# Kernel optimization log

Hardware: AMD Instinct MI355X
Metric: run time of the kernel (lower is better)

## Reference

```python
import jax, jax.numpy as jnp
import numpy as np

B, S, E, H = 32, 512, 512, 8
D = E // H  # head dim = 64
EPS = 1e-5


def setup_inputs() -> dict:
    key = jax.random.key(0)
    ks = jax.random.split(key, 6)
    x = jax.random.normal(ks[0], (B, S, E), dtype=jnp.float32)
    # nn.MultiheadAttention packed in-projection: [3E, E] weight, [3E] bias
    w_in = jax.random.normal(ks[1], (3 * E, E), dtype=jnp.float32) * 0.02
    b_in = jnp.zeros((3 * E,), dtype=jnp.float32)
    # out_proj: Linear(E, E)
    w_out = jax.random.normal(ks[2], (E, E), dtype=jnp.float32) * 0.02
    b_out = jnp.zeros((E,), dtype=jnp.float32)
    # LayerNorm(E) affine params
    gamma = jnp.ones((E,), dtype=jnp.float32)
    beta = jnp.zeros((E,), dtype=jnp.float32)
    return {"x": x, "w_in": w_in, "b_in": b_in, "w_out": w_out,
            "b_out": b_out, "gamma": gamma, "beta": beta}


def reference(x, w_in, b_in, w_out, b_out, gamma, beta):
    b, s, e = x.shape
    # packed QKV projection (torch: x @ W^T + b)
    qkv = x @ w_in.T + b_in                      # [B, S, 3E]
    q, k, v = jnp.split(qkv, 3, axis=-1)         # each [B, S, E]
    def to_heads(t):
        return t.reshape(b, s, H, D).transpose(0, 2, 1, 3)  # [B, H, S, D]
    q, k, v = to_heads(q), to_heads(k), to_heads(v)
    scores = jnp.einsum("bhqd,bhkd->bhqk", q, k) / jnp.sqrt(jnp.float32(D))
    att_w = jax.nn.softmax(scores, axis=-1)      # [B, H, S, S] per-head weights
    z = jnp.einsum("bhqk,bhkd->bhqd", att_w, v)  # [B, H, S, D]
    z = z.transpose(0, 2, 1, 3).reshape(b, s, e) # merge heads
    z = z @ w_out.T + b_out                      # out projection
    z = z + x                                    # residual connection
    # LayerNorm over last dim
    mu = jnp.mean(z, axis=-1, keepdims=True)
    var = jnp.var(z, axis=-1, keepdims=True)
    y = (z - mu) * jax.lax.rsqrt(var + EPS) * gamma + beta
    return (y, att_w)
```

## Files before the change

kernel.cpp:

```cpp
#include <hip/hip_runtime.h>
#include <hip/hip_bf16.h>
#include <stdint.h>

#define Bb 32
#define Ss 512
#define Ee 512
#define Hh 8
#define Dd 64
#define EPSf 1e-5f

typedef __attribute__((ext_vector_type(8))) unsigned short ushort8_t;
typedef __attribute__((ext_vector_type(4))) unsigned short ushort4_t;
typedef __attribute__((ext_vector_type(4))) float f32x4;
typedef __attribute__((ext_vector_type(4))) unsigned int uint4_t;
typedef __attribute__((ext_vector_type(8))) __bf16 bf16x8;

union U8cast { ushort8_t u; bf16x8 b; uint4_t w; };
__device__ __forceinline__ bf16x8 as_bf16x8(ushort8_t u) { U8cast c; c.u = u; return c.b; }
__device__ __forceinline__ bf16x8 words_bf16x8(unsigned int w0, unsigned int w1,
                                               unsigned int w2, unsigned int w3) {
  U8cast c; c.w = (uint4_t){w0, w1, w2, w3}; return c.b;
}

__device__ __forceinline__ unsigned short f2bf(float f) {
  __bf16 b = (__bf16)f;
  return __builtin_bit_cast(unsigned short, b);
}
__device__ __forceinline__ unsigned int pack2bf(float lo, float hi) {
  return ((unsigned int)f2bf(hi) << 16) | f2bf(lo);
}

__device__ __forceinline__ f32x4 mfma16(bf16x8 a, bf16x8 b, f32x4 c) {
  return __builtin_amdgcn_mfma_f32_16x16x32_bf16(a, b, c, 0, 0, 0);
}

__device__ __forceinline__ void async16(const unsigned short* g, unsigned short* l) {
  __builtin_amdgcn_global_load_lds(
      (const __attribute__((address_space(1))) void*)g,
      (__attribute__((address_space(3))) void*)l, 16, 0, 0);
}

__global__ __launch_bounds__(256) void cvt_bf16(const float* __restrict__ src,
                                                unsigned short* __restrict__ dst, int n8) {
  int i = blockIdx.x * 256 + threadIdx.x;
  int stride = gridDim.x * 256;
  for (; i < n8; i += stride) {
    float4 v0 = ((const float4*)src)[2 * i];
    float4 v1 = ((const float4*)src)[2 * i + 1];
    ushort8_t o;
    o[0] = f2bf(v0.x); o[1] = f2bf(v0.y); o[2] = f2bf(v0.z); o[3] = f2bf(v0.w);
    o[4] = f2bf(v1.x); o[5] = f2bf(v1.y); o[6] = f2bf(v1.z); o[7] = f2bf(v1.w);
    ((ushort8_t*)dst)[i] = o;
  }
}

__global__ __launch_bounds__(256) void qkv_mm(
    const unsigned short* __restrict__ Xb, const unsigned short* __restrict__ Wb,
    const float* __restrict__ bin,
    unsigned short* __restrict__ QL, unsigned short* __restrict__ KL,
    unsigned short* __restrict__ VL) {
  __shared__ unsigned short SH[128 * 128];
  unsigned short* As = SH;
  unsigned short* Bs = SH + 128 * 64;
  const int tid = threadIdx.x;
  const int w = tid >> 6, l = tid & 63;
  const int lr = l & 15, lg = l >> 4;
  const int id = blockIdx.x;
  const int gid = (id & 7) * 192 + (id >> 3);
  const int bx = gid % 12, by = gid / 12;
  const int m0 = by * 128, n0 = bx * 128;
  const int wm = (w >> 1) * 64, wn = (w & 1) * 64;
  f32x4 acc[4][4];
#pragma unroll
  for (int i = 0; i < 4; ++i)
#pragma unroll
    for (int j = 0; j < 4; ++j) acc[i][j] = (f32x4){0.f, 0.f, 0.f, 0.f};

  for (int k0 = 0; k0 < 512; k0 += 64) {
#pragma unroll
    for (int i = 0; i < 4; ++i) {
      int ci = (w * 4 + i) * 64 + l;
      int row = ci >> 3, kc = ci & 7;
      int gkc = kc ^ (row & 7);
      async16(Xb + (size_t)(m0 + row) * 512 + k0 + gkc * 8, &As[(w * 4 + i) * 512]);
      async16(Wb + (size_t)(n0 + row) * 512 + k0 + gkc * 8, &Bs[(w * 4 + i) * 512]);
    }
    __syncthreads();
#pragma unroll
    for (int ks = 0; ks < 2; ++ks) {
      bf16x8 af[4], bfr[4];
#pragma unroll
      for (int mf = 0; mf < 4; ++mf) {
        int row = wm + mf * 16 + lr;
        int gc = ks * 4 + lg;
        af[mf] = as_bf16x8(*(const ushort8_t*)&As[row * 64 + ((gc ^ (row & 7)) * 8)]);
      }
#pragma unroll
      for (int nf = 0; nf < 4; ++nf) {
        int row = wn + nf * 16 + lr;
        int gc = ks * 4 + lg;
        bfr[nf] = as_bf16x8(*(const ushort8_t*)&Bs[row * 64 + ((gc ^ (row & 7)) * 8)]);
      }
#pragma unroll
      for (int mf = 0; mf < 4; ++mf)
#pragma unroll
        for (int nf = 0; nf < 4; ++nf) acc[mf][nf] = mfma16(af[mf], bfr[nf], acc[mf][nf]);
    }
    __syncthreads();
  }

  const int which = n0 >> 9;
  const int bb = m0 >> 9, s0b = m0 & 511;
  const int h0 = (n0 & 511) >> 6;
#pragma unroll
  for (int nf = 0; nf < 4; ++nf) {
    int nl = wn + nf * 16 + lr;
    float bias = bin[n0 + nl];
#pragma unroll
    for (int mf = 0; mf < 4; ++mf) {
#pragma unroll
      for (int r = 0; r < 4; ++r) {
        int ml = wm + mf * 16 + lg * 4 + r;
        int row = (which == 2) ? nl : ml;
        int col = (which == 2) ? ml : nl;
        SH[row * 128 + ((((col >> 3) ^ (row & 7)) << 3) | (col & 7))] =
            f2bf(acc[mf][nf][r] + bias);
      }
    }
  }
  __syncthreads();

  unsigned short* dst = (which == 0) ? QL : (which == 1) ? KL : VL;
  const int frag0 = s0b >> 3;
#pragma unroll
  for (int i = 0; i < 8; ++i) {
    int c = tid + i * 256;
    int h_rel = c >> 10, cc = c & 1023;
    int fr = cc >> 6, ln = cc & 63;
    int row, col;
    if (which == 0) {
      row = (fr >> 1) * 16 + (ln & 15);
      col = h_rel * 64 + (fr & 1) * 32 + (ln >> 4) * 8;
    } else if (which == 1) {
      row = (fr >> 2) * 32 + ((fr >> 1) & 1) * 4 + ((ln & 15) >> 2) * 8 + (ln & 3);
      col = h_rel * 64 + (fr & 1) * 32 + (ln >> 4) * 8;
    } else {
      row = h_rel * 64 + (fr & 3) * 16 + (ln & 15);
      col = (fr >> 2) * 32 + (ln >> 4) * 8;
    }
    ushort8_t v = *(const ushort8_t*)&SH[row * 128 + (((col >> 3) ^ (row & 7)) << 3)];
    size_t base = (size_t)(bb * Hh + h0 + h_rel) * 32768;
    *(ushort8_t*)&dst[base + (size_t)(frag0 + fr) * 512 + ln * 8] = v;
  }
}

__global__ __launch_bounds__(256, 4) void attn_fused(
    const unsigned short* __restrict__ QL, const unsigned short* __restrict__ KL,
    const unsigned short* __restrict__ VL, float* __restrict__ att,
    unsigned short* __restrict__ Zb) {
  __shared__ unsigned short SH[2][8192];
  const int tid = threadIdx.x;
  const int w = tid >> 6, l = tid & 63;
  const int lr = l & 15, lg = l >> 4;
  const int id = blockIdx.x;
  const int bh = (id >> 6) * 8 + (id & 7);
  const int m0 = ((id >> 3) & 7) * 64;
  const int b = bh >> 3, h = bh & 7;
  const unsigned short* Qp = QL + (size_t)bh * 32768;
  const unsigned short* Kp = KL + (size_t)bh * 32768;
  const unsigned short* Vp = VL + (size_t)bh * 32768;

  const int qb = (m0 >> 4) + w;
  bf16x8 bq0 = as_bf16x8(*(const ushort8_t*)(Qp + (size_t)(qb * 2) * 512 + l * 8));
  bf16x8 bq1 = as_bf16x8(*(const ushort8_t*)(Qp + (size_t)(qb * 2 + 1) * 512 + l * 8));

#define STAGE_K(C, buf)                                                        \
  {                                                                            \
    _Pragma("unroll") for (int i = 0; i < 2; ++i)                              \
        async16(Kp + (size_t)(C)*4096 + (w * 2 + i) * 512 + l * 8,             \
                &SH[buf][(w * 2 + i) * 512]);                                  \
  }
#define STAGE_V(C, buf)                                                        \
  {                                                                            \
    _Pragma("unroll") for (int i = 0; i < 2; ++i)                              \
        async16(Vp + (size_t)(C)*4096 + (w * 2 + i) * 512 + l * 8,             \
                &SH[buf][4096 + (w * 2 + i) * 512]);                           \
  }

  float m_run = -1e30f, ssum = 0.f;
  STAGE_K(0, 0);
  __syncthreads();
#pragma unroll
  for (int C = 0; C < 8; ++C) {
    if (C < 7) STAGE_K(C + 1, (C + 1) & 1);
    f32x4 s4[4];
#pragma unroll
    for (int j = 0; j < 4; ++j) {
      bf16x8 ak0 = as_bf16x8(*(const ushort8_t*)&SH[C & 1][(2 * j) * 512 + l * 8]);
      bf16x8 ak1 = as_bf16x8(*(const ushort8_t*)&SH[C & 1][(2 * j + 1) * 512 + l * 8]);
      f32x4 z = (f32x4){0.f, 0.f, 0.f, 0.f};
      z = mfma16(ak0, bq0, z);
      s4[j] = mfma16(ak1, bq1, z);
    }
    float cm = s4[0][0];
#pragma unroll
    for (int j = 0; j < 4; ++j)
#pragma unroll
      for (int r = 0; r < 4; ++r) cm = fmaxf(cm, s4[j][r]);
    cm = fmaxf(cm, __shfl_xor(cm, 16));
    cm = fmaxf(cm, __shfl_xor(cm, 32));
    float nm = fmaxf(m_run, cm);
    ssum *= __expf((m_run - nm) * 0.125f);
    m_run = nm;
#pragma unroll
    for (int j = 0; j < 4; ++j) {
      float p0 = __expf((s4[j][0] - nm) * 0.125f);
      float p1 = __expf((s4[j][1] - nm) * 0.125f);
      float p2 = __expf((s4[j][2] - nm) * 0.125f);
      float p3 = __expf((s4[j][3] - nm) * 0.125f);
      ssum += (p0 + p1) + (p2 + p3);
    }
    __syncthreads();
  }
  ssum += __shfl_xor(ssum, 16);
  ssum += __shfl_xor(ssum, 32);
  const float inv = 1.0f / ssum;
  const float mfin = m_run;

  f32x4 o[4];
#pragma unroll
  for (int df = 0; df < 4; ++df) o[df] = (f32x4){0.f, 0.f, 0.f, 0.f};
  float* attb = att + (size_t)bh * Ss * Ss + (size_t)(m0 + w * 16) * Ss;
  const int dr8 = l >> 3, dc = l & 7;
  const int src0 = ((dc >> 1) << 4) + dr8;
  const int podd = dc & 1;

  STAGE_K(0, 0);
  STAGE_V(0, 0);
  __syncthreads();
#pragma unroll
  for (int C = 0; C < 8; ++C) {
    if (C < 7) {
      STAGE_K(C + 1, (C + 1) & 1);
      STAGE_V(C + 1, (C + 1) & 1);
    }
    f32x4 s4[4];
#pragma unroll
    for (int j = 0; j < 4; ++j) {
      bf16x8 ak0 = as_bf16x8(*(const ushort8_t*)&SH[C & 1][(2 * j) * 512 + l * 8]);
      bf16x8 ak1 = as_bf16x8(*(const ushort8_t*)&SH[C & 1][(2 * j + 1) * 512 + l * 8]);
      f32x4 z = (f32x4){0.f, 0.f, 0.f, 0.f};
      z = mfma16(ak0, bq0, z);
      s4[j] = mfma16(ak1, bq1, z);
    }
#pragma unroll
    for (int j = 0; j < 4; ++j)
#pragma unroll
      for (int r = 0; r < 4; ++r)
        s4[j][r] = __expf((s4[j][r] - mfin) * 0.125f) * inv;

#pragma unroll
    for (int cc = 0; cc < 2; ++cc) {
      int c2 = 2 * C + cc;
#pragma unroll
      for (int hh = 0; hh < 2; ++hh) {
        int srcl = src0 + hh * 8;
        f32x4 g;
        g[0] = __shfl(s4[2 * cc + podd][0], srcl, 64);
        g[1] = __shfl(s4[2 * cc + podd][1], srcl, 64);
        g[2] = __shfl(s4[2 * cc + podd][2], srcl, 64);
        g[3] = __shfl(s4[2 * cc + podd][3], srcl, 64);
        float* p = attb + (size_t)(hh * 8 + dr8) * Ss + c2 * 32 + dc * 4;
        __builtin_nontemporal_store(g, (f32x4*)p);
      }
      bf16x8 bp = words_bf16x8(pack2bf(s4[2 * cc][0], s4[2 * cc][1]),
                               pack2bf(s4[2 * cc][2], s4[2 * cc][3]),
                               pack2bf(s4[2 * cc + 1][0], s4[2 * cc + 1][1]),
                               pack2bf(s4[2 * cc + 1][2], s4[2 * cc + 1][3]));
#pragma unroll
      for (int df = 0; df < 4; ++df) {
        bf16x8 av = as_bf16x8(
            *(const ushort8_t*)&SH[C & 1][4096 + (cc * 4 + df) * 512 + l * 8]);
        o[df] = mfma16(av, bp, o[df]);
      }
    }
    __syncthreads();
  }

  unsigned short* zrow = Zb + ((size_t)(b * Ss) + m0 + w * 16 + lr) * Ee + h * Dd;
#pragma unroll
  for (int df = 0; df < 4; ++df) {
    ushort4_t zz;
    zz[0] = f2bf(o[df][0]); zz[1] = f2bf(o[df][1]);
    zz[2] = f2bf(o[df][2]); zz[3] = f2bf(o[df][3]);
    *(ushort4_t*)(zrow + df * 16 + lg * 4) = zz;
  }
#undef STAGE_K
#undef STAGE_V
}

__global__ __launch_bounds__(256) void out_mm(
    const unsigned short* __restrict__ Zb, const unsigned short* __restrict__ Wb,
    const float* __restrict__ bout, const float* __restrict__ X,
    float* __restrict__ Y) {
  __shared__ unsigned short As[128 * 64];
  __shared__ unsigned short Bs[128 * 64];
  const int tid = threadIdx.x;
  const int w = tid >> 6, l = tid & 63;
  const int lr = l & 15, lg = l >> 4;
  const int id = blockIdx.x;
  const int gid = (id & 7) * 64 + (id >> 3);
  const int m0 = (gid >> 2) * 128, n0 = (gid & 3) * 128;
  const int wm = (w >> 1) * 64, wn = (w & 1) * 64;
  f32x4 acc[4][4];
#pragma unroll
  for (int i = 0; i < 4; ++i)
#pragma unroll
    for (int j = 0; j < 4; ++j) acc[i][j] = (f32x4){0.f, 0.f, 0.f, 0.f};

  for (int k0 = 0; k0 < 512; k0 += 64) {
#pragma unroll
    for (int i = 0; i < 4; ++i) {
      int ci = (w * 4 + i) * 64 + l;
      int row = ci >> 3, kc = ci & 7;
      int gkc = kc ^ (row & 7);
      async16(Zb + (size_t)(m0 + row) * 512 + k0 + gkc * 8, &As[(w * 4 + i) * 512]);
      async16(Wb + (size_t)(n0 + row) * 512 + k0 + gkc * 8, &Bs[(w * 4 + i) * 512]);
    }
    __syncthreads();
#pragma unroll
    for (int ks = 0; ks < 2; ++ks) {
      bf16x8 af[4], bfr[4];
#pragma unroll
      for (int mf = 0; mf < 4; ++mf) {
        int row = wm + mf * 16 + lr;
        int gc = ks * 4 + lg;
        af[mf] = as_bf16x8(*(const ushort8_t*)&As[row * 64 + ((gc ^ (row & 7)) * 8)]);
      }
#pragma unroll
      for (int nf = 0; nf < 4; ++nf) {
        int row = wn + nf * 16 + lr;
        int gc = ks * 4 + lg;
        bfr[nf] = as_bf16x8(*(const ushort8_t*)&Bs[row * 64 + ((gc ^ (row & 7)) * 8)]);
      }
#pragma unroll
      for (int mf = 0; mf < 4; ++mf)
#pragma unroll
        for (int nf = 0; nf < 4; ++nf) acc[mf][nf] = mfma16(af[mf], bfr[nf], acc[mf][nf]);
    }
    __syncthreads();
  }

#pragma unroll
  for (int nf = 0; nf < 4; ++nf) {
    int n = n0 + wn + nf * 16 + lr;
    float bias = bout[n];
#pragma unroll
    for (int mf = 0; mf < 4; ++mf) {
#pragma unroll
      for (int r = 0; r < 4; ++r) {
        int m = m0 + wm + mf * 16 + lg * 4 + r;
        Y[(size_t)m * 512 + n] = acc[mf][nf][r] + bias + X[(size_t)m * 512 + n];
      }
    }
  }
}

__global__ __launch_bounds__(128) void ln_kernel(
    const float* __restrict__ Z2, const float* __restrict__ gamma,
    const float* __restrict__ beta, float* __restrict__ Y) {
  const int row = blockIdx.x;
  const int t = threadIdx.x;
  float4 v = *(const float4*)(Z2 + (size_t)row * 512 + t * 4);
  float sum = v.x + v.y + v.z + v.w;
  float sq = v.x * v.x + v.y * v.y + v.z * v.z + v.w * v.w;
#pragma unroll
  for (int off = 32; off; off >>= 1) {
    sum += __shfl_xor(sum, off);
    sq += __shfl_xor(sq, off);
  }
  __shared__ float s0[2], s1[2];
  int wv = t >> 6;
  if ((t & 63) == 0) { s0[wv] = sum; s1[wv] = sq; }
  __syncthreads();
  sum = s0[0] + s0[1];
  sq = s1[0] + s1[1];
  float mu = sum * (1.0f / 512.0f);
  float var = sq * (1.0f / 512.0f) - mu * mu;
  float rs = rsqrtf(var + EPSf);
  float4 g = *(const float4*)(gamma + t * 4);
  float4 be = *(const float4*)(beta + t * 4);
  float4 o;
  o.x = (v.x - mu) * rs * g.x + be.x;
  o.y = (v.y - mu) * rs * g.y + be.y;
  o.z = (v.z - mu) * rs * g.z + be.z;
  o.w = (v.w - mu) * rs * g.w + be.w;
  *(float4*)(Y + (size_t)row * 512 + t * 4) = o;
}

extern "C" void kernel_launch(void* const* d_in, const int* in_sizes, int n_in,
                              void* d_out, int out_size, void* d_ws, size_t ws_size,
                              hipStream_t stream) {
  const float* x = (const float*)d_in[0];
  const float* w_in = (const float*)d_in[1];
  const float* b_in = (const float*)d_in[2];
  const float* w_out = (const float*)d_in[3];
  const float* b_out = (const float*)d_in[4];
  const float* gamma = (const float*)d_in[5];
  const float* beta = (const float*)d_in[6];

  float* y = (float*)d_out;
  float* att = (float*)d_out + (size_t)Bb * Ss * Ee;

  char* ws = (char*)d_ws;
  const size_t NBH = (size_t)Bb * Hh * Ss * Dd;
  unsigned short* QLb   = (unsigned short*)ws;
  unsigned short* KLb   = QLb + NBH;
  unsigned short* VLb   = KLb + NBH;
  unsigned short* xb    = VLb + NBH;
  unsigned short* Zb    = xb;
  unsigned short* winb  = xb + NBH;
  unsigned short* woutb = winb + (size_t)3 * Ee * Ee;

  cvt_bf16<<<dim3(1024), 256, 0, stream>>>(x, xb, (int)(NBH / 8));
  cvt_bf16<<<dim3(384), 256, 0, stream>>>(w_in, winb, (int)(3 * Ee * Ee / 8));
  cvt_bf16<<<dim3(128), 256, 0, stream>>>(w_out, woutb, (int)(Ee * Ee / 8));
  qkv_mm<<<dim3(1536), 256, 0, stream>>>(xb, winb, b_in, QLb, KLb, VLb);
  attn_fused<<<dim3(2048), 256, 0, stream>>>(QLb, KLb, VLb, att, Zb);
  out_mm<<<dim3(512), 256, 0, stream>>>(Zb, woutb, b_out, x, y);
  ln_kernel<<<dim3(16384), 128, 0, stream>>>(y, gamma, beta, y);
}
```

Measured before the change: 169.2 us.

## Fuse LayerNorm into out-projection GEMM and merge conversion kernels

```diff
diff --git a/kernel.cpp b/kernel.cpp
--- a/kernel.cpp
+++ b/kernel.cpp
@@ -40,13 +40,22 @@
       (__attribute__((address_space(3))) void*)l, 16, 0, 0);
 }
 
-__global__ __launch_bounds__(256) void cvt_bf16(const float* __restrict__ src,
-                                                unsigned short* __restrict__ dst, int n8) {
+__global__ __launch_bounds__(256) void cvt_all(
+    const float* __restrict__ x, const float* __restrict__ win,
+    const float* __restrict__ wout, unsigned short* __restrict__ dst) {
+  const int NX = 1048576;
+  const int NW = 98304;
+  const int NT = NX + NW + 32768;
   int i = blockIdx.x * 256 + threadIdx.x;
   int stride = gridDim.x * 256;
-  for (; i < n8; i += stride) {
-    float4 v0 = ((const float4*)src)[2 * i];
-    float4 v1 = ((const float4*)src)[2 * i + 1];
+  for (; i < NT; i += stride) {
+    const float* s;
+    int off;
+    if (i < NX) { s = x; off = i; }
+    else if (i < NX + NW) { s = win; off = i - NX; }
+    else { s = wout; off = i - NX - NW; }
+    float4 v0 = ((const float4*)s)[2 * off];
+    float4 v1 = ((const float4*)s)[2 * off + 1];
     ushort8_t o;
     o[0] = f2bf(v0.x); o[1] = f2bf(v0.y); o[2] = f2bf(v0.z); o[3] = f2bf(v0.w);
     o[4] = f2bf(v1.x); o[5] = f2bf(v1.y); o[6] = f2bf(v1.z); o[7] = f2bf(v1.w);
@@ -299,103 +308,128 @@
 #undef STAGE_V
 }
 
-__global__ __launch_bounds__(256) void out_mm(
+__global__ __launch_bounds__(256) void out_ln(
     const unsigned short* __restrict__ Zb, const unsigned short* __restrict__ Wb,
     const float* __restrict__ bout, const float* __restrict__ X,
+    const float* __restrict__ gamma, const float* __restrict__ beta,
     float* __restrict__ Y) {
-  __shared__ unsigned short As[128 * 64];
-  __shared__ unsigned short Bs[128 * 64];
+  __shared__ unsigned short As[32 * 32];
+  __shared__ unsigned short Bs[512 * 32];
   const int tid = threadIdx.x;
   const int w = tid >> 6, l = tid & 63;
   const int lr = l & 15, lg = l >> 4;
   const int id = blockIdx.x;
   const int gid = (id & 7) * 64 + (id >> 3);
-  const int m0 = (gid >> 2) * 128, n0 = (gid & 3) * 128;
-  const int wm = (w >> 1) * 64, wn = (w & 1) * 64;
-  f32x4 acc[4][4];
-#pragma unroll
-  for (int i = 0; i < 4; ++i)
-#pragma unroll
-    for (int j = 0; j < 4; ++j) acc[i][j] = (f32x4){0.f, 0.f, 0.f, 0.f};
-
-  for (int k0 = 0; k0 < 512; k0 += 64) {
-#pragma unroll
-    for (int i = 0; i < 4; ++i) {
-      int ci = (w * 4 + i) * 64 + l;
-      int row = ci >> 3, kc = ci & 7;
-      int gkc = kc ^ (row & 7);
-      async16(Zb + (size_t)(m0 + row) * 512 + k0 + gkc * 8, &As[(w * 4 + i) * 512]);
-      async16(Wb + (size_t)(n0 + row) * 512 + k0 + gkc * 8, &Bs[(w * 4 + i) * 512]);
-    }
-    __syncthreads();
-#pragma unroll
-    for (int ks = 0; ks < 2; ++ks) {
-      bf16x8 af[4], bfr[4];
-#pragma unroll
-      for (int mf = 0; mf < 4; ++mf) {
-        int row = wm + mf * 16 + lr;
-        int gc = ks * 4 + lg;
-        af[mf] = as_bf16x8(*(const ushort8_t*)&As[row * 64 + ((gc ^ (row & 7)) * 8)]);
-      }
-#pragma unroll
-      for (int nf = 0; nf < 4; ++nf) {
-        int row = wn + nf * 16 + lr;
-        int gc = ks * 4 + lg;
-        bfr[nf] = as_bf16x8(*(const ushort8_t*)&Bs[row * 64 + ((gc ^ (row & 7)) * 8)]);
-      }
-#pragma unroll
-      for (int mf = 0; mf < 4; ++mf)
-#pragma unroll
-        for (int nf = 0; nf < 4; ++nf) acc[mf][nf] = mfma16(af[mf], bfr[nf], acc[mf][nf]);
-    }
-    __syncthreads();
-  }
-
-#pragma unroll
-  for (int nf = 0; nf < 4; ++nf) {
-    int n = n0 + wn + nf * 16 + lr;
+  const int m0 = gid * 32;
+  const int wn = w * 128;
+  f32x4 acc[2][8];
+#pragma unroll
+  for (int i = 0; i < 2; ++i)
+#pragma unroll
+    for (int j = 0; j < 8; ++j) acc[i][j] = (f32x4){0.f, 0.f, 0.f, 0.f};
+
+  for (int k0 = 0; k0 < 512; k0 += 32) {
+#pragma unroll
+    for (int i = 0; i < 8; ++i) {
+      int ci = tid + i * 256;
+      int row = ci >> 2, kc = ci & 3, gkc = kc ^ (row & 3);
+      async16(Wb + (size_t)row * 512 + k0 + gkc * 8, &Bs[ci * 8]);
+    }
+    if (tid < 128) {
+      int row = tid >> 2, kc = tid & 3, gkc = kc ^ (row & 3);
+      async16(Zb + (size_t)(m0 + row) * 512 + k0 + gkc * 8, &As[tid * 8]);
+    }
+    __syncthreads();
+    bf16x8 af[2], bfr[8];
+#pragma unroll
+    for (int mf = 0; mf < 2; ++mf) {
+      int row = mf * 16 + lr;
+      af[mf] = as_bf16x8(*(const ushort8_t*)&As[row * 32 + ((lg ^ (row & 3)) * 8)]);
+    }
+#pragma unroll
+    for (int nf = 0; nf < 8; ++nf) {
+      int row = wn + nf * 16 + lr;
+      bfr[nf] = as_bf16x8(*(const ushort8_t*)&Bs[row * 32 + ((lg ^ (row & 3)) * 8)]);
+    }
+#pragma unroll
+    for (int mf = 0; mf < 2; ++mf)
+#pragma unroll
+      for (int nf = 0; nf < 8; ++nf) acc[mf][nf] = mfma16(af[mf], bfr[nf], acc[mf][nf]);
+    __syncthreads();
+  }
+
+  float sum[2][4], sq[2][4];
+#pragma unroll
+  for (int mf = 0; mf < 2; ++mf)
+#pragma unroll
+    for (int r = 0; r < 4; ++r) { sum[mf][r] = 0.f; sq[mf][r] = 0.f; }
+#pragma unroll
+  for (int nf = 0; nf < 8; ++nf) {
+    int n = wn + nf * 16 + lr;
     float bias = bout[n];
 #pragma unroll
-    for (int mf = 0; mf < 4; ++mf) {
+    for (int mf = 0; mf < 2; ++mf)
 #pragma unroll
       for (int r = 0; r < 4; ++r) {
-        int m = m0 + wm + mf * 16 + lg * 4 + r;
-        Y[(size_t)m * 512 + n] = acc[mf][nf][r] + bias + X[(size_t)m * 512 + n];
-      }
-    }
-  }
-}
-
-__global__ __launch_bounds__(128) void ln_kernel(
-    const float* __restrict__ Z2, const float* __restrict__ gamma,
-    const float* __restrict__ beta, float* __restrict__ Y) {
-  const int row = blockIdx.x;
-  const int t = threadIdx.x;
-  float4 v = *(const float4*)(Z2 + (size_t)row * 512 + t * 4);
-  float sum = v.x + v.y + v.z + v.w;
-  float sq = v.x * v.x + v.y * v.y + v.z * v.z + v.w * v.w;
-#pragma unroll
-  for (int off = 32; off; off >>= 1) {
-    sum += __shfl_xor(sum, off);
-    sq += __shfl_xor(sq, off);
-  }
-  __shared__ float s0[2], s1[2];
-  int wv = t >> 6;
-  if ((t & 63) == 0) { s0[wv] = sum; s1[wv] = sq; }
+        int m = m0 + mf * 16 + lg * 4 + r;
+        float v = acc[mf][nf][r] + bias + X[(size_t)m * 512 + n];
+        acc[mf][nf][r] = v;
+        sum[mf][r] += v;
+        sq[mf][r] += v * v;
+      }
+  }
+#pragma unroll
+  for (int mask = 1; mask < 16; mask <<= 1) {
+#pragma unroll
+    for (int mf = 0; mf < 2; ++mf)
+#pragma unroll
+      for (int r = 0; r < 4; ++r) {
+        sum[mf][r] += __shfl_xor(sum[mf][r], mask);
+        sq[mf][r] += __shfl_xor(sq[mf][r], mask);
+      }
+  }
+  float* S = (float*)As;
+  if (lr == 0) {
+#pragma unroll
+    for (int mf = 0; mf < 2; ++mf)
+#pragma unroll
+      for (int r = 0; r < 4; ++r) {
+        int row = mf * 16 + lg * 4 + r;
+        S[(w * 32 + row) * 2] = sum[mf][r];
+        S[(w * 32 + row) * 2 + 1] = sq[mf][r];
+      }
+  }
   __syncthreads();
-  sum = s0[0] + s0[1];
-  sq = s1[0] + s1[1];
-  float mu = sum * (1.0f / 512.0f);
-  float var = sq * (1.0f / 512.0f) - mu * mu;
-  float rs = rsqrtf(var + EPSf);
-  float4 g = *(const float4*)(gamma + t * 4);
-  float4 be = *(const float4*)(beta + t * 4);
-  float4 o;
-  o.x = (v.x - mu) * rs * g.x + be.x;
-  o.y = (v.y - mu) * rs * g.y + be.y;
-  o.z = (v.z - mu) * rs * g.z + be.z;
-  o.w = (v.w - mu) * rs * g.w + be.w;
-  *(float4*)(Y + (size_t)row * 512 + t * 4) = o;
+  float musv[2][4], rssv[2][4];
+#pragma unroll
+  for (int mf = 0; mf < 2; ++mf)
+#pragma unroll
+    for (int r = 0; r < 4; ++r) {
+      int row = mf * 16 + lg * 4 + r;
+      float t = 0.f, t2 = 0.f;
+#pragma unroll
+      for (int ww = 0; ww < 4; ++ww) {
+        t += S[(ww * 32 + row) * 2];
+        t2 += S[(ww * 32 + row) * 2 + 1];
+      }
+      float mu = t * (1.0f / 512.0f);
+      float var = t2 * (1.0f / 512.0f) - mu * mu;
+      musv[mf][r] = mu;
+      rssv[mf][r] = rsqrtf(var + EPSf);
+    }
+#pragma unroll
+  for (int nf = 0; nf < 8; ++nf) {
+    int n = wn + nf * 16 + lr;
+    float g = gamma[n], be = beta[n];
+#pragma unroll
+    for (int mf = 0; mf < 2; ++mf)
+#pragma unroll
+      for (int r = 0; r < 4; ++r) {
+        int m = m0 + mf * 16 + lg * 4 + r;
+        Y[(size_t)m * 512 + n] =
+            (acc[mf][nf][r] - musv[mf][r]) * rssv[mf][r] * g + be;
+      }
+  }
 }
 
 extern "C" void kernel_launch(void* const* d_in, const int* in_sizes, int n_in,
@@ -422,11 +456,8 @@
   unsigned short* winb  = xb + NBH;
   unsigned short* woutb = winb + (size_t)3 * Ee * Ee;
 
-  cvt_bf16<<<dim3(1024), 256, 0, stream>>>(x, xb, (int)(NBH / 8));
-  cvt_bf16<<<dim3(384), 256, 0, stream>>>(w_in, winb, (int)(3 * Ee * Ee / 8));
-  cvt_bf16<<<dim3(128), 256, 0, stream>>>(w_out, woutb, (int)(Ee * Ee / 8));
+  cvt_all<<<dim3(1024), 256, 0, stream>>>(x, w_in, w_out, xb);
   qkv_mm<<<dim3(1536), 256, 0, stream>>>(xb, winb, b_in, QLb, KLb, VLb);
   attn_fused<<<dim3(2048), 256, 0, stream>>>(QLb, KLb, VLb, att, Zb);
-  out_mm<<<dim3(512), 256, 0, stream>>>(Zb, woutb, b_out, x, y);
-  ln_kernel<<<dim3(16384), 128, 0, stream>>>(y, gamma, beta, y);
-}
+  out_ln<<<dim3(512), 256, 0, stream>>>(Zb, woutb, b_out, x, gamma, beta, y);
+}
```

After: 162.6 us. 3.9% less time.
